# Optimization experiments

Hardware: AMD Instinct MI355X
Metric: run time of the kernel (lower is better)

The kernel has to match this reference:

```python
import jax, jax.numpy as jnp
import numpy as np

EMBED_DIM = 1024
NUM_HEADS = 16
HEAD_DIM = EMBED_DIM // NUM_HEADS  # 64
TOKEN_GRID = 48
TASK_ROPE_TOKENS = 8
SEQ_LEN = TASK_ROPE_TOKENS + TOKEN_GRID * TOKEN_GRID  # 2312
ROT_DIM = HEAD_DIM // 2  # 32, rotary 'dim' arg
SCALE = HEAD_DIM ** -0.5


def _make_rope_tables():
    # Faithful to RotaryEmbedding.__init__
    freqs = 1.0 / 10000.0 ** (jnp.arange(0, ROT_DIM, 2, dtype=jnp.float32) / float(ROT_DIM))
    t = jnp.arange(TOKEN_GRID, dtype=jnp.float32) / float(TOKEN_GRID) * float(TOKEN_GRID)
    freqs_1d = jnp.einsum('i,f->if', t, freqs)          # [G, ROT_DIM/2]
    freqs_1d = jnp.repeat(freqs_1d, 2, axis=-1)          # [G, ROT_DIM]
    fh = jnp.broadcast_to(freqs_1d[:, None, :], (TOKEN_GRID, TOKEN_GRID, ROT_DIM))
    fw = jnp.broadcast_to(freqs_1d[None, :, :], (TOKEN_GRID, TOKEN_GRID, ROT_DIM))
    freqs_2d = jnp.concatenate([fh, fw], axis=-1)        # [G, G, HEAD_DIM]
    freqs_flat = freqs_2d.reshape(TOKEN_GRID * TOKEN_GRID, -1)
    return jnp.cos(freqs_flat), jnp.sin(freqs_flat)      # each [G*G, HEAD_DIM]


def _rotate_half(x):
    x1, x2 = jnp.split(x, 2, axis=-1)
    return jnp.concatenate([-x2, x1], axis=-1)


def _apply_rope(t, cos, sin):
    # t: [H, L, D]; rotate tokens after the task prefix
    usable = t.shape[1] - TASK_ROPE_TOKENS
    c = cos[:usable, :HEAD_DIM]
    s = sin[:usable, :HEAD_DIM]
    to_rotate = t[:, TASK_ROPE_TOKENS:, :HEAD_DIM]
    rotated = to_rotate * c + _rotate_half(to_rotate) * s
    prefix = t[:, :TASK_ROPE_TOKENS, :HEAD_DIM]
    return jnp.concatenate([prefix, rotated], axis=1)


def setup_inputs() -> dict:
    key = jax.random.key(0)
    k1, k2, k3, k4, k5 = jax.random.split(key, 5)
    cos, sin = _make_rope_tables()
    bound = 1.0 / np.sqrt(EMBED_DIM)
    return {
        'x': jax.random.normal(k1, (SEQ_LEN, EMBED_DIM), dtype=jnp.float32),
        'key_padding_mask': jnp.ones((SEQ_LEN,), dtype=bool),
        'qkv_w': jax.random.uniform(k2, (3 * EMBED_DIM, EMBED_DIM), minval=-bound, maxval=bound, dtype=jnp.float32),
        'qkv_b': jax.random.uniform(k3, (3 * EMBED_DIM,), minval=-bound, maxval=bound, dtype=jnp.float32),
        'proj_w': jax.random.uniform(k4, (EMBED_DIM, EMBED_DIM), minval=-bound, maxval=bound, dtype=jnp.float32),
        'proj_b': jax.random.uniform(k5, (EMBED_DIM,), minval=-bound, maxval=bound, dtype=jnp.float32),
        'freqs_cos': cos,
        'freqs_sin': sin,
    }


def reference(x, key_padding_mask, qkv_w, qkv_b, proj_w, proj_b, freqs_cos, freqs_sin):
    L = x.shape[0]
    qkv = x @ qkv_w.T + qkv_b                             # [L, 3E]
    qkv = qkv.reshape(L, 3, NUM_HEADS, HEAD_DIM)
    qkv = jnp.transpose(qkv, (1, 2, 0, 3))                # [3, H, L, D]
    q, k, v = qkv[0], qkv[1], qkv[2]
    q = _apply_rope(q, freqs_cos, freqs_sin)
    k = _apply_rope(k, freqs_cos, freqs_sin)
    scores = jnp.einsum('hld,hmd->hlm', q, k) * SCALE     # [H, L, L]
    scores = jnp.where(key_padding_mask[None, None, :], scores, jnp.finfo(scores.dtype).min)
    weights = jax.nn.softmax(scores, axis=-1)
    context = jnp.einsum('hij,hjd->hid', weights, v)      # [H, L, D]
    context = jnp.transpose(context, (1, 0, 2)).reshape(L, -1)  # [L, E]
    out = context @ proj_w.T + proj_b
    return out
```

## Files before the change

kernel.cpp:

```cpp
#include <hip/hip_runtime.h>
#include <hip/hip_bf16.h>

#define SEQ   2312
#define EMB   1024
#define NH    16
#define HD    64
#define LP    2368
#define NKT   37
#define KSPLIT0 19
#define QKVN  3072
#define QSCALE 0.1803368801111713f

typedef __bf16 bf16x8 __attribute__((ext_vector_type(8)));
typedef __bf16 bf16x4 __attribute__((ext_vector_type(4)));
typedef _Float16 f16x8 __attribute__((ext_vector_type(8)));
typedef _Float16 f16x4 __attribute__((ext_vector_type(4)));
typedef float  f32x4  __attribute__((ext_vector_type(4)));

#define MFMA16(a,b,c) __builtin_amdgcn_mfma_f32_16x16x32_bf16((a),(b),(c),0,0,0)

__global__ __launch_bounds__(256) void cast_bf16_kernel(const float* __restrict__ in,
                                                        __bf16* __restrict__ out, int n4) {
  int i = blockIdx.x * 256 + threadIdx.x;
  if (i < n4) {
    const float4 v = reinterpret_cast<const float4*>(in)[i];
    bf16x4 o = { (__bf16)v.x, (__bf16)v.y, (__bf16)v.z, (__bf16)v.w };
    reinterpret_cast<bf16x4*>(out)[i] = o;
  }
}

__device__ __forceinline__ bf16x8 lds_frag(const __bf16* __restrict__ buf, int row, int cb) {
  const char* p = (const char*)buf + row * 128 + (cb ^ ((row & 7) << 4));
  return *reinterpret_cast<const bf16x8*>(p);
}

__device__ __forceinline__ void gl_lds16(const char* g, char* l) {
  __builtin_amdgcn_global_load_lds(
      (const __attribute__((address_space(1))) void*)g,
      (__attribute__((address_space(3))) void*)l, 16, 0, 0);
}

template <bool OUT_BF16>
__global__ __launch_bounds__(256) void gemm_lds_kernel(const __bf16* __restrict__ A,
                                                       const __bf16* __restrict__ B,
                                                       const float* __restrict__ bias,
                                                       void* __restrict__ Cout,
                                                       int M, int N, int K, int MT) {
  const int g = ((int)blockIdx.x & 7) * ((int)gridDim.x >> 3) + ((int)blockIdx.x >> 3);
  const int mt = g % MT, nt = g / MT;
  const int t = threadIdx.x;
  const int wid = t >> 6;
  const int lane = t & 63;
  const int lr = lane & 15, lg = lane >> 4;
  const int mrow = (wid >> 1) * 64, ncol = (wid & 1) * 64;

  __shared__ __bf16 sbuf[2][2][128 * 64];

  const int srow = t >> 3;
  const int ksw  = ((t & 7) ^ (srow & 7)) * 8;
  const __bf16* asrc[4]; const __bf16* bsrc[4];
#pragma unroll
  for (int i = 0; i < 4; ++i) {
    const int row = i * 32 + srow;
    int arow = mt * 128 + row; if (arow >= M) arow = M - 1;
    asrc[i] = A + (size_t)arow * K + ksw;
    bsrc[i] = B + (size_t)(nt * 128 + row) * K + ksw;
  }

  auto issue = [&](int buf, int kk) {
    char* ab = (char*)sbuf[buf][0] + wid * 1024;
    char* bb = (char*)sbuf[buf][1] + wid * 1024;
#pragma unroll
    for (int i = 0; i < 4; ++i) gl_lds16((const char*)(asrc[i] + kk), ab + i * 4096);
#pragma unroll
    for (int i = 0; i < 4; ++i) gl_lds16((const char*)(bsrc[i] + kk), bb + i * 4096);
  };

  f32x4 acc[4][4] = {};
  const int NK = K >> 6;
  issue(0, 0);

  for (int ks = 0; ks < NK; ++ks) {
    asm volatile("s_waitcnt vmcnt(0)" ::: "memory");
    __syncthreads();
    if (ks + 1 < NK) issue((ks + 1) & 1, (ks + 1) << 6);
    const __bf16* ab = sbuf[ks & 1][0];
    const __bf16* bb = sbuf[ks & 1][1];
#pragma unroll
    for (int kh2 = 0; kh2 < 2; ++kh2) {
      bf16x8 af[4], bf[4];
#pragma unroll
      for (int m = 0; m < 4; ++m) af[m] = lds_frag(ab, mrow + m * 16 + lr, kh2 * 64 + lg * 16);
#pragma unroll
      for (int n = 0; n < 4; ++n) bf[n] = lds_frag(bb, ncol + n * 16 + lr, kh2 * 64 + lg * 16);
#pragma unroll
      for (int m = 0; m < 4; ++m)
#pragma unroll
        for (int n = 0; n < 4; ++n)
          acc[m][n] = MFMA16(af[m], bf[n], acc[m][n]);
    }
    __syncthreads();
  }

#pragma unroll
  for (int m = 0; m < 4; ++m) {
#pragma unroll
    for (int n = 0; n < 4; ++n) {
#pragma unroll
      for (int r = 0; r < 4; ++r) {
        int row = mt * 128 + mrow + m * 16 + lg * 4 + r;
        int col = nt * 128 + ncol + n * 16 + lr;
        if (row < M) {
          float v = acc[m][n][r] + bias[col];
          if (OUT_BF16) reinterpret_cast<__bf16*>(Cout)[(size_t)row * N + col] = (__bf16)v;
          else          reinterpret_cast<float*>(Cout)[(size_t)row * N + col] = v;
        }
      }
    }
  }
}

__global__ __launch_bounds__(256) void gemm_qkv_kernel(const __bf16* __restrict__ A,
                                                       const __bf16* __restrict__ B,
                                                       const float* __restrict__ bias,
                                                       const float* __restrict__ fcos,
                                                       const float* __restrict__ fsin,
                                                       __bf16* __restrict__ qh,
                                                       __bf16* __restrict__ kh,
                                                       __bf16* __restrict__ vt) {
  const int g = ((int)blockIdx.x & 7) * 57 + ((int)blockIdx.x >> 3);
  const int mt = g % 19, nt = g / 19;
  const int t = threadIdx.x;
  const int wid = t >> 6;
  const int lane = t & 63;
  const int lr = lane & 15, lg = lane >> 4;
  const int mrow = (wid >> 1) * 64, ncol = (wid & 1) * 64;

  __shared__ __bf16 sbuf[2][2][128 * 64];

  const int srow = t >> 3;
  const int ksw  = ((t & 7) ^ (srow & 7)) * 8;
  const __bf16* asrc[4]; const __bf16* bsrc[4];
#pragma unroll
  for (int i = 0; i < 4; ++i) {
    const int row = i * 32 + srow;
    int arow = mt * 128 + row; if (arow >= SEQ) arow = SEQ - 1;
    asrc[i] = A + (size_t)arow * EMB + ksw;
    bsrc[i] = B + (size_t)(nt * 128 + row) * EMB + ksw;
  }

  auto issue = [&](int buf, int kk) {
    char* ab = (char*)sbuf[buf][0] + wid * 1024;
    char* bb = (char*)sbuf[buf][1] + wid * 1024;
#pragma unroll
    for (int i = 0; i < 4; ++i) gl_lds16((const char*)(asrc[i] + kk), ab + i * 4096);
#pragma unroll
    for (int i = 0; i < 4; ++i) gl_lds16((const char*)(bsrc[i] + kk), bb + i * 4096);
  };

  f32x4 acc[4][4] = {};
  issue(0, 0);

  for (int ks = 0; ks < 16; ++ks) {
    asm volatile("s_waitcnt vmcnt(0)" ::: "memory");
    __syncthreads();
    if (ks + 1 < 16) issue((ks + 1) & 1, (ks + 1) << 6);
    const __bf16* ab = sbuf[ks & 1][0];
    const __bf16* bb = sbuf[ks & 1][1];
#pragma unroll
    for (int kh2 = 0; kh2 < 2; ++kh2) {
      bf16x8 af[4], bf[4];
#pragma unroll
      for (int m = 0; m < 4; ++m) af[m] = lds_frag(ab, mrow + m * 16 + lr, kh2 * 64 + lg * 16);
#pragma unroll
      for (int n = 0; n < 4; ++n) bf[n] = lds_frag(bb, ncol + n * 16 + lr, kh2 * 64 + lg * 16);
#pragma unroll
      for (int m = 0; m < 4; ++m)
#pragma unroll
        for (int n = 0; n < 4; ++n)
          acc[m][n] = MFMA16(af[m], bf[n], acc[m][n]);
    }
    __syncthreads();
  }

  const int colbase = nt * 128 + ncol;
  const int hb   = colbase >> 6;
  const int kind = hb >> 4;
  const int h    = hb & 15;
  float bb4[4];
#pragma unroll
  for (int n = 0; n < 4; ++n) bb4[n] = bias[colbase + n * 16 + lr];

  if (kind < 2) {
    __bf16* dst = (kind == 0 ? qh : kh) + (size_t)h * LP * 64;
    const float sc = (kind == 0) ? QSCALE : 1.0f;
#pragma unroll
    for (int m = 0; m < 4; ++m) {
#pragma unroll
      for (int r = 0; r < 4; ++r) {
        const int row = mt * 128 + mrow + m * 16 + lg * 4 + r;
        if (row >= SEQ) continue;
        float v0 = acc[m][0][r] + bb4[0];
        float v1 = acc[m][1][r] + bb4[1];
        float v2 = acc[m][2][r] + bb4[2];
        float v3 = acc[m][3][r] + bb4[3];
        if (row >= 8) {
          const float* cr = fcos + (size_t)(row - 8) * 64;
          const float* sr = fsin + (size_t)(row - 8) * 64;
          const float c0 = cr[lr],      s0 = sr[lr];
          const float c1 = cr[16 + lr], s1 = sr[16 + lr];
          const float c2 = cr[32 + lr], s2 = sr[32 + lr];
          const float c3 = cr[48 + lr], s3 = sr[48 + lr];
          const float o0 = v0 * c0 - v2 * s0;
          const float o2 = v2 * c2 + v0 * s2;
          const float o1 = v1 * c1 - v3 * s1;
          const float o3 = v3 * c3 + v1 * s3;
          v0 = o0; v1 = o1; v2 = o2; v3 = o3;
        }
        __bf16* p = dst + (size_t)row * 64;
        p[lr]      = (__bf16)(v0 * sc);
        p[16 + lr] = (__bf16)(v1 * sc);
        p[32 + lr] = (__bf16)(v2 * sc);
        p[48 + lr] = (__bf16)(v3 * sc);
      }
    }
  } else {
    __syncthreads();
    __bf16 (*vtile)[66] =
        reinterpret_cast<__bf16(*)[66]>((__bf16*)sbuf + wid * 64 * 66);
#pragma unroll
    for (int m = 0; m < 4; ++m)
#pragma unroll
      for (int r = 0; r < 4; ++r) {
        const int rl = m * 16 + lg * 4 + r;
#pragma unroll
        for (int n = 0; n < 4; ++n)
          vtile[rl][n * 16 + lr] = (__bf16)(acc[m][n][r] + bb4[n]);
      }
    __builtin_amdgcn_wave_barrier();
    const int prow0 = mt * 128 + mrow;
    const int pos = prow0 + lane;
    __bf16* vdst = vt + (size_t)h * 64 * LP;
    if (pos < LP) {
#pragma unroll 4
      for (int dl = 0; dl < 64; ++dl)
        vdst[(size_t)dl * LP + pos] = vtile[lane][dl];
    }
  }
}

__global__ __launch_bounds__(256) void flash_kernel(const __bf16* __restrict__ qh,
                                                    const __bf16* __restrict__ kh,
                                                    const __bf16* __restrict__ vt,
                                                    _Float16* __restrict__ Op,
                                                    float* __restrict__ lp) {
  const int g = (blockIdx.x & 7) * 148 + (blockIdx.x >> 3);
  const int h = g / 74;
  const int rem = g - h * 74;
  const int qb = rem >> 1, sp = rem & 1;
  const int kt0 = sp ? KSPLIT0 : 0, ktend = sp ? NKT : KSPLIT0;
  const int t = threadIdx.x;
  const int wid = t >> 6;
  const int lane = t & 63;
  const int lr = lane & 15, lg = lane >> 4;
  const int q0 = qb * 64 + wid * 16;

  __shared__ __bf16 kbuf[64 * 64];
  __shared__ __bf16 vbuf[64 * 64];
  __shared__ __bf16 plds[4][16][72];

  const __bf16* qbase = qh + ((size_t)h * LP + q0) * HD;
  const bf16x8 aq0 = *reinterpret_cast<const bf16x8*>(qbase + lr * HD + lg * 8);
  const bf16x8 aq1 = *reinterpret_cast<const bf16x8*>(qbase + lr * HD + 32 + lg * 8);

  const __bf16* khead = kh + (size_t)h * LP * HD;
  const __bf16* vhead = vt + (size_t)h * HD * LP;

  const int krow0 = t >> 3,        kcb0 = (t & 7) * 16;
  const int krow1 = 32 + (t >> 3);
  const int vrow  = t >> 2,        vcb0 = (t & 3) * 32;
  const int koff0 = krow0 * 128 + (kcb0 ^ ((krow0 & 7) << 4));
  const int koff1 = krow1 * 128 + (kcb0 ^ ((krow1 & 7) << 4));
  const int voff0 = vrow * 128 + (vcb0 ^ ((vrow & 7) << 4));
  const int voff1 = vrow * 128 + ((vcb0 + 16) ^ ((vrow & 7) << 4));
  const __bf16* vsrc = vhead + (size_t)vrow * LP + (t & 3) * 16;

  bf16x8 kreg0, kreg1, vreg0, vreg1;
  auto stage_load = [&](int kt) {
    const __bf16* kb = khead + (size_t)kt * 64 * HD;
    kreg0 = *reinterpret_cast<const bf16x8*>(kb + t * 8);
    kreg1 = *reinterpret_cast<const bf16x8*>(kb + 2048 + t * 8);
    vreg0 = *reinterpret_cast<const bf16x8*>(vsrc + kt * 64);
    vreg1 = *reinterpret_cast<const bf16x8*>(vsrc + kt * 64 + 8);
  };

  float l = 0.f;
  f32x4 oacc[4] = {};

  stage_load(kt0);

  for (int kt = kt0; kt < ktend; ++kt) {
    __syncthreads();
    *reinterpret_cast<bf16x8*>((char*)kbuf + koff0) = kreg0;
    *reinterpret_cast<bf16x8*>((char*)kbuf + koff1) = kreg1;
    *reinterpret_cast<bf16x8*>((char*)vbuf + voff0) = vreg0;
    *reinterpret_cast<bf16x8*>((char*)vbuf + voff1) = vreg1;
    __syncthreads();
    if (kt + 1 < ktend) stage_load(kt + 1);

    f32x4 sacc[4] = {};
    __builtin_amdgcn_s_setprio(1);
#pragma unroll
    for (int cg = 0; cg < 4; ++cg) {
      sacc[cg] = MFMA16(lds_frag(kbuf, cg * 16 + lr, lg * 16),      aq0, sacc[cg]);
      sacc[cg] = MFMA16(lds_frag(kbuf, cg * 16 + lr, 64 + lg * 16), aq1, sacc[cg]);
    }
    __builtin_amdgcn_s_setprio(0);
    if (kt == NKT - 1) {
#pragma unroll
      for (int cg = 0; cg < 4; ++cg)
#pragma unroll
        for (int r = 0; r < 4; ++r)
          if (kt * 64 + cg * 16 + lg * 4 + r >= SEQ) sacc[cg][r] = -1e30f;
    }
#pragma unroll
    for (int cg = 0; cg < 4; ++cg)
#pragma unroll
      for (int r = 0; r < 4; ++r) sacc[cg][r] = exp2f(sacc[cg][r]);
    float s0 = (sacc[0][0] + sacc[0][1]) + (sacc[0][2] + sacc[0][3]);
    float s1 = (sacc[1][0] + sacc[1][1]) + (sacc[1][2] + sacc[1][3]);
    float s2 = (sacc[2][0] + sacc[2][1]) + (sacc[2][2] + sacc[2][3]);
    float s3 = (sacc[3][0] + sacc[3][1]) + (sacc[3][2] + sacc[3][3]);
    l += (s0 + s1) + (s2 + s3);
#pragma unroll
    for (int cg = 0; cg < 4; ++cg) {
      bf16x4 pk = { (__bf16)sacc[cg][0], (__bf16)sacc[cg][1],
                    (__bf16)sacc[cg][2], (__bf16)sacc[cg][3] };
      *reinterpret_cast<bf16x4*>(&plds[wid][lr][cg * 16 + lg * 4]) = pk;
    }
    __builtin_amdgcn_wave_barrier();
    const bf16x8 ap0 = *reinterpret_cast<const bf16x8*>(&plds[wid][lr][lg * 8]);
    const bf16x8 ap1 = *reinterpret_cast<const bf16x8*>(&plds[wid][lr][32 + lg * 8]);
    __builtin_amdgcn_s_setprio(1);
#pragma unroll
    for (int cg = 0; cg < 4; ++cg) {
      oacc[cg] = MFMA16(lds_frag(vbuf, cg * 16 + lr, lg * 16),      ap0, oacc[cg]);
      oacc[cg] = MFMA16(lds_frag(vbuf, cg * 16 + lr, 64 + lg * 16), ap1, oacc[cg]);
    }
    __builtin_amdgcn_s_setprio(0);
  }
  float ltot = l;
  ltot += __shfl_xor(ltot, 16, 64);
  ltot += __shfl_xor(ltot, 32, 64);
  const float inv = 1.0f / ltot;
  const size_t rbase = ((size_t)sp * NH + h) * LP;
  if (lg == 0) lp[rbase + q0 + lr] = ltot;
  _Float16* orow = Op + (rbase + q0 + lr) * 64 + lg * 4;
#pragma unroll
  for (int cg = 0; cg < 4; ++cg) {
    f16x4 ov = { (_Float16)(oacc[cg][0] * inv), (_Float16)(oacc[cg][1] * inv),
                 (_Float16)(oacc[cg][2] * inv), (_Float16)(oacc[cg][3] * inv) };
    *reinterpret_cast<f16x4*>(orow + cg * 16) = ov;
  }
}

__global__ __launch_bounds__(256) void merge_kernel(const _Float16* __restrict__ Op,
                                                    const float* __restrict__ lp,
                                                    __bf16* __restrict__ ctx) {
  const int tg = blockIdx.x * 256 + threadIdx.x;
  const int rid = tg >> 2;
  const int d0 = (tg & 3) << 4;
  const int h = rid / LP;
  const int row = rid - h * LP;
  if (row >= SEQ) return;
  const size_t i0 = (size_t)h * LP + row;
  const size_t i1 = (size_t)NH * LP + i0;
  float w0 = lp[i0], w1 = lp[i1];
  const float inv = 1.0f / (w0 + w1);
  w0 *= inv; w1 *= inv;
  const f16x8* o0 = reinterpret_cast<const f16x8*>(Op + i0 * 64 + d0);
  const f16x8* o1 = reinterpret_cast<const f16x8*>(Op + i1 * 64 + d0);
  __bf16* co = ctx + (size_t)row * EMB + h * 64 + d0;
#pragma unroll
  for (int v = 0; v < 2; ++v) {
    const f16x8 a = o0[v], b = o1[v];
    bf16x8 o;
#pragma unroll
    for (int j = 0; j < 8; ++j)
      o[j] = (__bf16)((float)a[j] * w0 + (float)b[j] * w1);
    reinterpret_cast<bf16x8*>(co)[v] = o;
  }
}

extern "C" void kernel_launch(void* const* d_in, const int* in_sizes, int n_in,
                              void* d_out, int out_size, void* d_ws, size_t ws_size,
                              hipStream_t stream) {
  const float* x      = (const float*)d_in[0];
  const float* qkv_w  = (const float*)d_in[2];
  const float* qkv_b  = (const float*)d_in[3];
  const float* proj_w = (const float*)d_in[4];
  const float* proj_b = (const float*)d_in[5];
  const float* fcos   = (const float*)d_in[6];
  const float* fsin   = (const float*)d_in[7];
  float* out = (float*)d_out;

  char* ws = (char*)d_ws;
  size_t off = 0;
  auto alloc = [&](size_t bytes) {
    char* p = ws + off;
    off += (bytes + 255) & ~size_t(255);
    return p;
  };
  __bf16* xb     = (__bf16*)alloc((size_t)SEQ * EMB * 2);
  __bf16* wqkvb  = (__bf16*)alloc((size_t)QKVN * EMB * 2);
  __bf16* wprojb = (__bf16*)alloc((size_t)EMB * EMB * 2);
  __bf16* qh     = (__bf16*)alloc((size_t)NH * LP * HD * 2);
  __bf16* kh     = (__bf16*)alloc((size_t)NH * LP * HD * 2);
  __bf16* vtr    = (__bf16*)alloc((size_t)NH * HD * LP * 2);
  __bf16* ctx    = (__bf16*)alloc((size_t)SEQ * EMB * 2);
  _Float16* Op   = (_Float16*)alloc((size_t)2 * NH * LP * 64 * 2);
  float*    lpv  = (float*)alloc((size_t)2 * NH * LP * 4);

  cast_bf16_kernel<<<(SEQ * EMB / 4 + 255) / 256, 256, 0, stream>>>(x, xb, SEQ * EMB / 4);
  cast_bf16_kernel<<<(QKVN * EMB / 4 + 255) / 256, 256, 0, stream>>>(qkv_w, wqkvb, QKVN * EMB / 4);
  cast_bf16_kernel<<<(EMB * EMB / 4 + 255) / 256, 256, 0, stream>>>(proj_w, wprojb, EMB * EMB / 4);

  gemm_qkv_kernel<<<456, 256, 0, stream>>>(xb, wqkvb, qkv_b, fcos, fsin, qh, kh, vtr);
  flash_kernel<<<1184, 256, 0, stream>>>(qh, kh, vtr, Op, lpv);
  merge_kernel<<<592, 256, 0, stream>>>(Op, lpv, ctx);
  gemm_lds_kernel<false><<<152, 256, 0, stream>>>(ctx, wprojb, proj_b, out,
                                                  SEQ, EMB, EMB, 19);
}
```

Measured before the change: 121.1 us.

## Merge weight casts into one launch and enlarge QKV GEMM tile to 256x128

The three fp32-to-bf16 cast launches become a single kernel that picks source and destination by index range, which removes two launch gaps. The QKV projection GEMM moves from 128x128 tiles with 256 threads to 256x128 tiles with 512 threads (8 waves), so each B tile is reused across more rows and the grid shrinks from 456 to 240 blocks. The trade-off is fewer blocks than before on 256 CUs, larger LDS use per block (96KB), and a last M tile that is mostly padding (2312 rows over 10 tiles of 256).

```diff
diff --git a/kernel.cpp b/kernel.cpp
--- a/kernel.cpp
+++ b/kernel.cpp
@@ -19,14 +19,25 @@
 
 #define MFMA16(a,b,c) __builtin_amdgcn_mfma_f32_16x16x32_bf16((a),(b),(c),0,0,0)
 
-__global__ __launch_bounds__(256) void cast_bf16_kernel(const float* __restrict__ in,
-                                                        __bf16* __restrict__ out, int n4) {
+#define N1 (SEQ * EMB / 4)
+#define N2 (QKVN * EMB / 4)
+#define N3 (EMB * EMB / 4)
+
+__global__ __launch_bounds__(256) void cast_all_kernel(const float* __restrict__ x,
+                                                       const float* __restrict__ qkv_w,
+                                                       const float* __restrict__ proj_w,
+                                                       __bf16* __restrict__ xb,
+                                                       __bf16* __restrict__ wqkvb,
+                                                       __bf16* __restrict__ wprojb) {
   int i = blockIdx.x * 256 + threadIdx.x;
-  if (i < n4) {
-    const float4 v = reinterpret_cast<const float4*>(in)[i];
-    bf16x4 o = { (__bf16)v.x, (__bf16)v.y, (__bf16)v.z, (__bf16)v.w };
-    reinterpret_cast<bf16x4*>(out)[i] = o;
-  }
+  const float* src; __bf16* dst; int j;
+  if (i < N1)           { src = x;      dst = xb;     j = i; }
+  else if (i < N1 + N2) { src = qkv_w;  dst = wqkvb;  j = i - N1; }
+  else if (i < N1 + N2 + N3) { src = proj_w; dst = wprojb; j = i - N1 - N2; }
+  else return;
+  const float4 v = reinterpret_cast<const float4*>(src)[j];
+  bf16x4 o = { (__bf16)v.x, (__bf16)v.y, (__bf16)v.z, (__bf16)v.w };
+  reinterpret_cast<bf16x4*>(dst)[j] = o;
 }
 
 __device__ __forceinline__ bf16x8 lds_frag(const __bf16* __restrict__ buf, int row, int cb) {
@@ -120,7 +131,7 @@
   }
 }
 
-__global__ __launch_bounds__(256) void gemm_qkv_kernel(const __bf16* __restrict__ A,
+__global__ __launch_bounds__(512) void gemm_qkv_kernel(const __bf16* __restrict__ A,
                                                        const __bf16* __restrict__ B,
                                                        const float* __restrict__ bias,
                                                        const float* __restrict__ fcos,
@@ -128,34 +139,36 @@
                                                        __bf16* __restrict__ qh,
                                                        __bf16* __restrict__ kh,
                                                        __bf16* __restrict__ vt) {
-  const int g = ((int)blockIdx.x & 7) * 57 + ((int)blockIdx.x >> 3);
-  const int mt = g % 19, nt = g / 19;
+  const int g = ((int)blockIdx.x & 7) * 30 + ((int)blockIdx.x >> 3);
+  const int mt = g % 10, nt = g / 10;
   const int t = threadIdx.x;
   const int wid = t >> 6;
   const int lane = t & 63;
   const int lr = lane & 15, lg = lane >> 4;
-  const int mrow = (wid >> 1) * 64, ncol = (wid & 1) * 64;
-
-  __shared__ __bf16 sbuf[2][2][128 * 64];
+  const int mrow = (wid >> 1) * 64;
+  const int ncol = (wid & 1) * 64;
+
+  __shared__ __bf16 smem[49152];
 
   const int srow = t >> 3;
   const int ksw  = ((t & 7) ^ (srow & 7)) * 8;
-  const __bf16* asrc[4]; const __bf16* bsrc[4];
+  const __bf16* asrc[4]; const __bf16* bsrc[2];
 #pragma unroll
   for (int i = 0; i < 4; ++i) {
-    const int row = i * 32 + srow;
-    int arow = mt * 128 + row; if (arow >= SEQ) arow = SEQ - 1;
+    int arow = mt * 256 + i * 64 + srow; if (arow >= SEQ) arow = SEQ - 1;
     asrc[i] = A + (size_t)arow * EMB + ksw;
-    bsrc[i] = B + (size_t)(nt * 128 + row) * EMB + ksw;
-  }
+  }
+#pragma unroll
+  for (int i = 0; i < 2; ++i)
+    bsrc[i] = B + (size_t)(nt * 128 + i * 64 + srow) * EMB + ksw;
 
   auto issue = [&](int buf, int kk) {
-    char* ab = (char*)sbuf[buf][0] + wid * 1024;
-    char* bb = (char*)sbuf[buf][1] + wid * 1024;
-#pragma unroll
-    for (int i = 0; i < 4; ++i) gl_lds16((const char*)(asrc[i] + kk), ab + i * 4096);
-#pragma unroll
-    for (int i = 0; i < 4; ++i) gl_lds16((const char*)(bsrc[i] + kk), bb + i * 4096);
+    char* ab = (char*)(smem + buf * 16384) + wid * 1024;
+    char* bb = (char*)(smem + 32768 + buf * 8192) + wid * 1024;
+#pragma unroll
+    for (int i = 0; i < 4; ++i) gl_lds16((const char*)(asrc[i] + kk), ab + i * 8192);
+#pragma unroll
+    for (int i = 0; i < 2; ++i) gl_lds16((const char*)(bsrc[i] + kk), bb + i * 8192);
   };
 
   f32x4 acc[4][4] = {};
@@ -165,8 +178,8 @@
     asm volatile("s_waitcnt vmcnt(0)" ::: "memory");
     __syncthreads();
     if (ks + 1 < 16) issue((ks + 1) & 1, (ks + 1) << 6);
-    const __bf16* ab = sbuf[ks & 1][0];
-    const __bf16* bb = sbuf[ks & 1][1];
+    const __bf16* ab = smem + (ks & 1) * 16384;
+    const __bf16* bb = smem + 32768 + (ks & 1) * 8192;
 #pragma unroll
     for (int kh2 = 0; kh2 < 2; ++kh2) {
       bf16x8 af[4], bf[4];
@@ -198,7 +211,7 @@
     for (int m = 0; m < 4; ++m) {
 #pragma unroll
       for (int r = 0; r < 4; ++r) {
-        const int row = mt * 128 + mrow + m * 16 + lg * 4 + r;
+        const int row = mt * 256 + mrow + m * 16 + lg * 4 + r;
         if (row >= SEQ) continue;
         float v0 = acc[m][0][r] + bb4[0];
         float v1 = acc[m][1][r] + bb4[1];
@@ -226,8 +239,7 @@
     }
   } else {
     __syncthreads();
-    __bf16 (*vtile)[66] =
-        reinterpret_cast<__bf16(*)[66]>((__bf16*)sbuf + wid * 64 * 66);
+    __bf16 (*vtile)[66] = reinterpret_cast<__bf16(*)[66]>(smem + wid * 64 * 66);
 #pragma unroll
     for (int m = 0; m < 4; ++m)
 #pragma unroll
@@ -238,8 +250,7 @@
           vtile[rl][n * 16 + lr] = (__bf16)(acc[m][n][r] + bb4[n]);
       }
     __builtin_amdgcn_wave_barrier();
-    const int prow0 = mt * 128 + mrow;
-    const int pos = prow0 + lane;
+    const int pos = mt * 256 + mrow + lane;
     __bf16* vdst = vt + (size_t)h * 64 * LP;
     if (pos < LP) {
 #pragma unroll 4
@@ -421,11 +432,10 @@
   _Float16* Op   = (_Float16*)alloc((size_t)2 * NH * LP * 64 * 2);
   float*    lpv  = (float*)alloc((size_t)2 * NH * LP * 4);
 
-  cast_bf16_kernel<<<(SEQ * EMB / 4 + 255) / 256, 256, 0, stream>>>(x, xb, SEQ * EMB / 4);
-  cast_bf16_kernel<<<(QKVN * EMB / 4 + 255) / 256, 256, 0, stream>>>(qkv_w, wqkvb, QKVN * EMB / 4);
-  cast_bf16_kernel<<<(EMB * EMB / 4 + 255) / 256, 256, 0, stream>>>(proj_w, wprojb, EMB * EMB / 4);
-
-  gemm_qkv_kernel<<<456, 256, 0, stream>>>(xb, wqkvb, qkv_b, fcos, fsin, qh, kh, vtr);
+  cast_all_kernel<<<(N1 + N2 + N3 + 255) / 256, 256, 0, stream>>>(
+      x, qkv_w, proj_w, xb, wqkvb, wprojb);
+
+  gemm_qkv_kernel<<<240, 512, 0, stream>>>(xb, wqkvb, qkv_b, fcos, fsin, qh, kh, vtr);
   flash_kernel<<<1184, 256, 0, stream>>>(qh, kh, vtr, Op, lpv);
   merge_kernel<<<592, 256, 0, stream>>>(Op, lpv, ctx);
   gemm_lds_kernel<false><<<152, 256, 0, stream>>>(ctx, wprojb, proj_b, out,
```

After: 114.7 us. 5.3% less time.
